# Kernel tuning notes

Hardware: AMD Instinct MI355X
Metric: run time of the kernel (lower is better)

The kernel has to match this reference:

```python
import jax, jax.numpy as jnp
import numpy as np

N, E, D_IN, D_OUT = 50000, 800000, 128, 128


def setup_inputs() -> dict:
    key = jax.random.key(0)
    ks = jax.random.split(key, 16)
    # edges with no self-loops (add_remaining_self_loops then simply appends one loop per node)
    row = jax.random.randint(ks[0], (E,), 0, N, dtype=jnp.int32)
    off = jax.random.randint(ks[1], (E,), 1, N, dtype=jnp.int32)
    col = (row + off) % N
    edge_index = jnp.stack([row, col], axis=0)
    s_in = 1.0 / np.sqrt(D_IN)
    s_out = 1.0 / np.sqrt(D_OUT)
    u = lambda k, shape, s: jax.random.uniform(k, shape, jnp.float32, -s, s)
    return {
        "x": jax.random.normal(ks[2], (N, D_IN), jnp.float32),
        "edge_index": edge_index,
        "W_hp": u(ks[3], (D_OUT, D_IN), s_in), "b_hp": u(ks[4], (D_OUT,), s_in),
        "W_lp": u(ks[5], (D_OUT, D_IN), s_in), "b_lp": u(ks[6], (D_OUT,), s_in),
        "W_i": u(ks[7], (D_OUT, D_IN), s_in), "b_i": u(ks[8], (D_OUT,), s_in),
        "wlin_h": u(ks[9], (D_OUT,), s_out), "blin_h": u(ks[10], (), s_out),
        "wlin_l": u(ks[11], (D_OUT,), s_out), "blin_l": u(ks[12], (), s_out),
        "wlin_i": u(ks[13], (D_OUT,), s_out), "blin_i": u(ks[14], (), s_out),
    }


def reference(x, edge_index, W_hp, b_hp, W_lp, b_lp, W_i, b_i,
              wlin_h, blin_h, wlin_l, blin_l, wlin_i, blin_i):
    n = x.shape[0]
    row, col = edge_index[0], edge_index[1]
    loop = jnp.arange(n, dtype=row.dtype)
    rf = jnp.concatenate([row, loop])  # sources incl. self-loops
    cf = jnp.concatenate([col, loop])  # targets incl. self-loops
    w = jnp.ones(rf.shape[0], x.dtype)
    # symmetric GCN normalization: D^{-1/2} A_hat D^{-1/2}
    deg = jax.ops.segment_sum(w, cf, num_segments=n)
    dinv = jnp.where(deg > 0, deg ** -0.5, 0.0).astype(x.dtype)
    w = dinv[rf] * w * dinv[cf]

    def agg(h):  # out[i] = sum_j w_e * h[j] over edges j->i
        return jax.ops.segment_sum(w[:, None] * h[rf], cf, num_segments=n)

    h_hp = x @ W_hp.T + b_hp
    H_hp = jax.nn.relu(h_hp - agg(h_hp))          # high-pass
    h_lp = x @ W_lp.T + b_lp
    H_lp = jax.nn.relu(agg(h_lp))                 # low-pass
    H_i = jax.nn.relu(x @ W_i.T + b_i)            # identity

    a_h = jax.nn.sigmoid(H_hp @ wlin_h + blin_h)  # [N]
    a_l = jax.nn.sigmoid(H_lp @ wlin_l + blin_l)
    a_i = jax.nn.sigmoid(H_i @ wlin_i + blin_i)
    # diag(alpha) @ H == alpha[:, None] * H
    return a_h[:, None] * H_hp + a_l[:, None] * H_lp + a_i[:, None] * H_i
```

## Files before the change

kernel.cpp:

```cpp
#include <hip/hip_runtime.h>
#include <cstdint>
#include <cstddef>

#define DEV __device__ __forceinline__

typedef __bf16 bf16x8 __attribute__((ext_vector_type(8)));
typedef float f32x4 __attribute__((ext_vector_type(4)));
typedef unsigned short ushort8v __attribute__((ext_vector_type(8)));

DEV ushort f2b(float f) {
  uint u = __float_as_uint(f);
  return (ushort)((u + 0x7FFFu + ((u >> 16) & 1u)) >> 16);
}

DEV ushort4 cvt4(float4 v) {
  ushort4 o; o.x = f2b(v.x); o.y = f2b(v.y); o.z = f2b(v.z); o.w = f2b(v.w);
  return o;
}

DEV float4 shfl_xor4(float4 v, int m) {
  float4 r;
  r.x = __shfl_xor(v.x, m); r.y = __shfl_xor(v.y, m);
  r.z = __shfl_xor(v.z, m); r.w = __shfl_xor(v.w, m);
  return r;
}

DEV float4 unpack4(uint2 u) {
  float4 r;
  r.x = __uint_as_float(u.x << 16);
  r.y = __uint_as_float(u.x & 0xFFFF0000u);
  r.z = __uint_as_float(u.y << 16);
  r.w = __uint_as_float(u.y & 0xFFFF0000u);
  return r;
}

DEV void fma4(float4& a, float w, uint2 u) {
  float4 v = unpack4(u);
  a.x = fmaf(w, v.x, a.x); a.y = fmaf(w, v.y, a.y);
  a.z = fmaf(w, v.z, a.z); a.w = fmaf(w, v.w, a.w);
}

__global__ __launch_bounds__(256) void k_count_cvtw(
    const int* __restrict__ col, int* __restrict__ cnt, int E, int nCB,
    const float* __restrict__ W0, const float* __restrict__ W1,
    const float* __restrict__ W2, ushort* __restrict__ Wb) {
  int b = blockIdx.x;
  if (b >= nCB) {
    int mi = b - nCB;
    const float* src = (mi == 0) ? W0 : (mi == 1) ? W1 : W2;
    ushort* dst = Wb + mi * 16384;
    for (int i = threadIdx.x * 4; i < 16384; i += 1024)
      *(ushort4*)(dst + i) = cvt4(*(const float4*)(src + i));
    return;
  }
  int e = b * 256 + threadIdx.x;
  if (e < E) atomicAdd(&cnt[col[e]], 1);
}

__global__ __launch_bounds__(256) void k_scanA(const int* __restrict__ cnt,
                                               int* __restrict__ off,
                                               float* __restrict__ dinv,
                                               int* __restrict__ btot, int N) {
  __shared__ int ws[4];
  int t = threadIdx.x, ln = t & 63, wv = t >> 6;
  int i = blockIdx.x * 256 + t;
  int v = (i < N) ? cnt[i] : 0;
  int inc = v;
#pragma unroll
  for (int o = 1; o < 64; o <<= 1) {
    int u = __shfl_up(inc, o);
    if (ln >= o) inc += u;
  }
  if (ln == 63) ws[wv] = inc;
  __syncthreads();
  if (t == 0) {
    int s = 0;
#pragma unroll
    for (int w = 0; w < 4; ++w) { int tmp = ws[w]; ws[w] = s; s += tmp; }
  }
  __syncthreads();
  int excl = ws[wv] + inc - v;
  if (i < N) {
    off[i] = excl;
    dinv[i] = rsqrtf((float)v + 1.0f);
  }
  if (t == 255) btot[blockIdx.x] = excl + v;
}

__global__ __launch_bounds__(256) void k_scanBC(int* __restrict__ off,
                                                const int* __restrict__ btot,
                                                int* __restrict__ cursor,
                                                int N, int E, int NB) {
  __shared__ int ws[4];
  __shared__ int pre_sh[256];
  int t = threadIdx.x, ln = t & 63, wv = t >> 6;
  int v = (t < NB) ? btot[t] : 0;
  int inc = v;
#pragma unroll
  for (int o = 1; o < 64; o <<= 1) {
    int u = __shfl_up(inc, o);
    if (ln >= o) inc += u;
  }
  if (ln == 63) ws[wv] = inc;
  __syncthreads();
  if (t == 0) {
    int s = 0;
#pragma unroll
    for (int w = 0; w < 4; ++w) { int tmp = ws[w]; ws[w] = s; s += tmp; }
  }
  __syncthreads();
  pre_sh[t] = ws[wv] + inc - v;
  __syncthreads();
  int bpre = pre_sh[blockIdx.x];
  int i = blockIdx.x * 256 + t;
  if (i < N) {
    int o = off[i] + bpre;
    off[i] = o;
    cursor[i] = o;
  }
  if (blockIdx.x == 0 && t == 0) off[N] = E;
}

__global__ __launch_bounds__(256) void k_scatter(const int* __restrict__ ei,
                                                 const float* __restrict__ dinv,
                                                 int* __restrict__ cursor,
                                                 int2* __restrict__ edata, int E) {
  int e = blockIdx.x * 256 + threadIdx.x;
  if (e >= E) return;
  int s = ei[e], d = ei[E + e];
  float w = dinv[s] * dinv[d];
  int p = atomicAdd(&cursor[d], 1);
  int2 v; v.x = s; v.y = __float_as_int(w);
  edata[p] = v;
}

__global__ __launch_bounds__(512) void k_gemm_fused(
    const float* __restrict__ x, const ushort* __restrict__ Wb,
    const float* __restrict__ b_hp, const float* __restrict__ b_lp,
    const float* __restrict__ b_i,
    ushort* __restrict__ h_all, int N) {
  __shared__ ushort Wl[16384];
  int tid = (int)threadIdx.x, lane = tid & 63, wv = tid >> 6;
  int r = lane & 15, g = lane >> 4;
  int NT = N >> 4;
  int t = blockIdx.x * 8 + wv;
  bool active = t < NT;

  bf16x8 Af[4];
  if (active) {
    const float* xp = x + ((size_t)t * 16 + r) * 128 + g * 8;
#pragma unroll
    for (int kc = 0; kc < 4; ++kc) {
      float4 v0 = *(const float4*)(xp + kc * 32);
      float4 v1 = *(const float4*)(xp + kc * 32 + 4);
      ushort8v u;
      u[0] = f2b(v0.x); u[1] = f2b(v0.y); u[2] = f2b(v0.z); u[3] = f2b(v0.w);
      u[4] = f2b(v1.x); u[5] = f2b(v1.y); u[6] = f2b(v1.z); u[7] = f2b(v1.w);
      Af[kc] = __builtin_bit_cast(bf16x8, u);
    }
  }

  for (int m = 0; m < 3; ++m) {
    __syncthreads();
    for (int i = tid; i < 2048; i += 512) {
      int byte = i << 4;
      int row = byte >> 8;
      int swz = byte ^ ((row & 7) << 4);
      *(ushort8v*)((char*)Wl + swz) = *(const ushort8v*)(Wb + m * 16384 + (i << 3));
    }
    __syncthreads();
    if (!active) continue;
    const float* bias = (m == 0) ? b_hp : (m == 1) ? b_lp : b_i;
    f32x4 acc[8];
#pragma unroll
    for (int ct = 0; ct < 8; ++ct) {
      float bb = bias[ct * 16 + r];
      f32x4 c; c[0] = bb; c[1] = bb; c[2] = bb; c[3] = bb;
      acc[ct] = c;
    }
#pragma unroll
    for (int kc = 0; kc < 4; ++kc)
#pragma unroll
      for (int ct = 0; ct < 8; ++ct) {
        int row = ct * 16 + r;
        int byte = row * 256 + kc * 64 + g * 16;
        int swz = byte ^ ((row & 7) << 4);
        bf16x8 B = *(const bf16x8*)((const char*)Wl + swz);
        acc[ct] = __builtin_amdgcn_mfma_f32_16x16x32_bf16(Af[kc], B, acc[ct], 0, 0, 0);
      }
    ushort* op = h_all + (size_t)(t * 16 + g * 4) * 384 + m * 128 + r;
#pragma unroll
    for (int ct = 0; ct < 8; ++ct)
#pragma unroll
      for (int j = 0; j < 4; ++j) {
        float v = acc[ct][j];
        if (m == 2) v = fmaxf(v, 0.f);
        op[(size_t)j * 384 + ct * 16] = f2b(v);
      }
  }
}

__global__ __launch_bounds__(256) void k_agg_final(
    const ushort* __restrict__ h_all, const float* __restrict__ dinv,
    const int* __restrict__ off, const int2* __restrict__ edata,
    const float* __restrict__ wlh, const float* __restrict__ wll,
    const float* __restrict__ wli,
    const float* __restrict__ pbh, const float* __restrict__ pbl,
    const float* __restrict__ pbi,
    float* __restrict__ out, int N) {
  int wv = (int)threadIdx.x >> 6;
  int lane = (int)threadIdx.x & 63;
  int node = blockIdx.x * 4 + wv;
  if (node >= N) return;

  const ushort* hb = h_all + 4 * lane;
  int p0 = off[node], p1 = off[node + 1];

  float4 a0 = {0,0,0,0}, a1 = {0,0,0,0}, a2 = {0,0,0,0}, a3 = {0,0,0,0};
  int p = p0;
  for (; p + 4 <= p1; p += 4) {
    int2 e0 = edata[p], e1 = edata[p + 1], e2 = edata[p + 2], e3 = edata[p + 3];
    uint2 u0 = *(const uint2*)(const void*)(hb + (size_t)e0.x * 384);
    uint2 u1 = *(const uint2*)(const void*)(hb + (size_t)e1.x * 384);
    uint2 u2 = *(const uint2*)(const void*)(hb + (size_t)e2.x * 384);
    uint2 u3 = *(const uint2*)(const void*)(hb + (size_t)e3.x * 384);
    fma4(a0, __int_as_float(e0.y), u0);
    fma4(a1, __int_as_float(e1.y), u1);
    fma4(a2, __int_as_float(e2.y), u2);
    fma4(a3, __int_as_float(e3.y), u3);
  }
  for (; p < p1; ++p) {
    int2 e = edata[p];
    uint2 u = *(const uint2*)(const void*)(hb + (size_t)e.x * 384);
    fma4(a0, __int_as_float(e.y), u);
  }
  float4 own;
  own.x = (a0.x + a1.x) + (a2.x + a3.x);
  own.y = (a0.y + a1.y) + (a2.y + a3.y);
  own.z = (a0.z + a1.z) + (a2.z + a3.z);
  own.w = (a0.w + a1.w) + (a2.w + a3.w);

  float di = dinv[node], wself = di * di;
  float4 sv = unpack4(*(const uint2*)(const void*)(hb + (size_t)node * 384));
  own.x = fmaf(wself, sv.x, own.x); own.y = fmaf(wself, sv.y, own.y);
  own.z = fmaf(wself, sv.z, own.z); own.w = fmaf(wself, sv.w, own.w);

  float4 oth = shfl_xor4(own, 32);
  float4 svo = shfl_xor4(sv, 32);
  bool hpside = (lane < 32);
  float4 hpSelf, aggHp, aggLp;
  hpSelf.x = hpside ? sv.x : svo.x; hpSelf.y = hpside ? sv.y : svo.y;
  hpSelf.z = hpside ? sv.z : svo.z; hpSelf.w = hpside ? sv.w : svo.w;
  aggHp.x = hpside ? own.x : oth.x; aggHp.y = hpside ? own.y : oth.y;
  aggHp.z = hpside ? own.z : oth.z; aggHp.w = hpside ? own.w : oth.w;
  aggLp.x = hpside ? oth.x : own.x; aggLp.y = hpside ? oth.y : own.y;
  aggLp.z = hpside ? oth.z : own.z; aggLp.w = hpside ? oth.w : own.w;

  float4 Hh, Hl;
  Hh.x = fmaxf(hpSelf.x - aggHp.x, 0.f); Hh.y = fmaxf(hpSelf.y - aggHp.y, 0.f);
  Hh.z = fmaxf(hpSelf.z - aggHp.z, 0.f); Hh.w = fmaxf(hpSelf.w - aggHp.w, 0.f);
  Hl.x = fmaxf(aggLp.x, 0.f); Hl.y = fmaxf(aggLp.y, 0.f);
  Hl.z = fmaxf(aggLp.z, 0.f); Hl.w = fmaxf(aggLp.w, 0.f);

  int c4 = 4 * (lane & 31);
  float4 hi4 = unpack4(*(const uint2*)(const void*)(h_all + (size_t)node * 384 + 256 + c4));
  float4 wh = *(const float4*)(wlh + c4);
  float4 wl = *(const float4*)(wll + c4);
  float4 wi = *(const float4*)(wli + c4);

  float dh = Hh.x * wh.x + Hh.y * wh.y + Hh.z * wh.z + Hh.w * wh.w;
  float dl = Hl.x * wl.x + Hl.y * wl.y + Hl.z * wl.z + Hl.w * wl.w;
  float dd = hi4.x * wi.x + hi4.y * wi.y + hi4.z * wi.z + hi4.w * wi.w;
#pragma unroll
  for (int o = 32; o > 0; o >>= 1) {
    dh += __shfl_xor(dh, o);
    dl += __shfl_xor(dl, o);
    dd += __shfl_xor(dd, o);
  }
  float a_h = 1.f / (1.f + __expf(-(0.5f * dh + pbh[0])));
  float a_l = 1.f / (1.f + __expf(-(0.5f * dl + pbl[0])));
  float a_i = 1.f / (1.f + __expf(-(0.5f * dd + pbi[0])));

  if (hpside) {
    float4 o4;
    o4.x = a_h * Hh.x + a_l * Hl.x + a_i * hi4.x;
    o4.y = a_h * Hh.y + a_l * Hl.y + a_i * hi4.y;
    o4.z = a_h * Hh.z + a_l * Hl.z + a_i * hi4.z;
    o4.w = a_h * Hh.w + a_l * Hl.w + a_i * hi4.w;
    *(float4*)(out + (size_t)node * 128 + c4) = o4;
  }
}

extern "C" void kernel_launch(void* const* d_in, const int* in_sizes, int n_in,
                              void* d_out, int out_size, void* d_ws, size_t ws_size,
                              hipStream_t stream) {
  const float* x     = (const float*)d_in[0];
  const int*   ei    = (const int*)d_in[1];
  const float* W_hp  = (const float*)d_in[2];
  const float* b_hp  = (const float*)d_in[3];
  const float* W_lp  = (const float*)d_in[4];
  const float* b_lp  = (const float*)d_in[5];
  const float* W_i   = (const float*)d_in[6];
  const float* b_i   = (const float*)d_in[7];
  const float* wlh   = (const float*)d_in[8];
  const float* pbh   = (const float*)d_in[9];
  const float* wll   = (const float*)d_in[10];
  const float* pbl   = (const float*)d_in[11];
  const float* wli   = (const float*)d_in[12];
  const float* pbi   = (const float*)d_in[13];
  float* out = (float*)d_out;

  int N = in_sizes[0] / 128;
  int E = in_sizes[1] / 2;
  int NB = (N + 255) / 256;
  int nCB = (E + 255) / 256;

  ushort* h_all = (ushort*)d_ws;
  ushort* Wb    = h_all + (size_t)N * 384;
  int2*   edata = (int2*)(Wb + 3 * 16384);
  float*  dinv  = (float*)(edata + E);
  int*    cnt   = (int*)(dinv + N);
  int*    off   = cnt + N;
  int*    cursor= off + N + 1;
  int*    btot  = cursor + N;

  hipMemsetAsync(cnt, 0, sizeof(int) * N, stream);
  k_count_cvtw<<<nCB + 3, 256, 0, stream>>>(ei + E, cnt, E, nCB, W_hp, W_lp, W_i, Wb);
  k_scanA<<<NB, 256, 0, stream>>>(cnt, off, dinv, btot, N);
  k_scanBC<<<NB, 256, 0, stream>>>(off, btot, cursor, N, E, NB);
  k_scatter<<<(E + 255) / 256, 256, 0, stream>>>(ei, dinv, cursor, edata, E);
  k_gemm_fused<<<(N / 16 + 7) / 8, 512, 0, stream>>>(x, Wb, b_hp, b_lp, b_i, h_all, N);
  k_agg_final<<<(N + 3) / 4, 256, 0, stream>>>(
      h_all, dinv, off, edata, wlh, wll, wli, pbh, pbl, pbi, out, N);
}
```

Measured before the change: 264.9 us.

## Fold weight conversion and count zeroing into GEMM, unroll aggregation by eight

Each GEMM block now converts the fp32 weights to bf16 itself while staging them into shared memory, and the GEMM also zeroes the degree-count array. This removes the memset and the separate weight-conversion blocks, and the GEMM is moved to the front of the launch sequence. The aggregation loop is unrolled from four to eight edges per iteration with more accumulators, to keep more gathers in flight, and the wave index is made scalar with readfirstlane. In exchange, every GEMM block redoes the weight conversion, and the extra accumulators raise register pressure.

```diff
diff --git a/kernel.cpp b/kernel.cpp
--- a/kernel.cpp
+++ b/kernel.cpp
@@ -11,11 +11,6 @@
 DEV ushort f2b(float f) {
   uint u = __float_as_uint(f);
   return (ushort)((u + 0x7FFFu + ((u >> 16) & 1u)) >> 16);
-}
-
-DEV ushort4 cvt4(float4 v) {
-  ushort4 o; o.x = f2b(v.x); o.y = f2b(v.y); o.z = f2b(v.z); o.w = f2b(v.w);
-  return o;
 }
 
 DEV float4 shfl_xor4(float4 v, int m) {
@@ -40,20 +35,90 @@
   a.z = fmaf(w, v.z, a.z); a.w = fmaf(w, v.w, a.w);
 }
 
-__global__ __launch_bounds__(256) void k_count_cvtw(
-    const int* __restrict__ col, int* __restrict__ cnt, int E, int nCB,
+__global__ __launch_bounds__(512) void k_gemm_fused(
+    const float* __restrict__ x,
     const float* __restrict__ W0, const float* __restrict__ W1,
-    const float* __restrict__ W2, ushort* __restrict__ Wb) {
-  int b = blockIdx.x;
-  if (b >= nCB) {
-    int mi = b - nCB;
-    const float* src = (mi == 0) ? W0 : (mi == 1) ? W1 : W2;
-    ushort* dst = Wb + mi * 16384;
-    for (int i = threadIdx.x * 4; i < 16384; i += 1024)
-      *(ushort4*)(dst + i) = cvt4(*(const float4*)(src + i));
-    return;
-  }
-  int e = b * 256 + threadIdx.x;
+    const float* __restrict__ W2,
+    const float* __restrict__ b_hp, const float* __restrict__ b_lp,
+    const float* __restrict__ b_i,
+    ushort* __restrict__ h_all, int* __restrict__ cnt, int N) {
+  int tid = (int)threadIdx.x;
+  {
+    int gsz = (int)gridDim.x * 512;
+    for (int i = (int)blockIdx.x * 512 + tid; i < N; i += gsz) cnt[i] = 0;
+  }
+
+  __shared__ ushort Wl[16384];
+  int lane = tid & 63, wv = tid >> 6;
+  int r = lane & 15, g = lane >> 4;
+  int NT = N >> 4;
+  int t = blockIdx.x * 8 + wv;
+  bool active = t < NT;
+
+  bf16x8 Af[4];
+  if (active) {
+    const float* xp = x + ((size_t)t * 16 + r) * 128 + g * 8;
+#pragma unroll
+    for (int kc = 0; kc < 4; ++kc) {
+      float4 v0 = *(const float4*)(xp + kc * 32);
+      float4 v1 = *(const float4*)(xp + kc * 32 + 4);
+      ushort8v u;
+      u[0] = f2b(v0.x); u[1] = f2b(v0.y); u[2] = f2b(v0.z); u[3] = f2b(v0.w);
+      u[4] = f2b(v1.x); u[5] = f2b(v1.y); u[6] = f2b(v1.z); u[7] = f2b(v1.w);
+      Af[kc] = __builtin_bit_cast(bf16x8, u);
+    }
+  }
+
+  for (int m = 0; m < 3; ++m) {
+    const float* Wsrc = (m == 0) ? W0 : (m == 1) ? W1 : W2;
+    __syncthreads();
+    for (int i = tid; i < 2048; i += 512) {
+      int byte = i << 4;
+      int row = byte >> 8;
+      int swz = byte ^ ((row & 7) << 4);
+      const float* s = Wsrc + (i << 3);
+      float4 v0 = *(const float4*)s;
+      float4 v1 = *(const float4*)(s + 4);
+      ushort8v u;
+      u[0] = f2b(v0.x); u[1] = f2b(v0.y); u[2] = f2b(v0.z); u[3] = f2b(v0.w);
+      u[4] = f2b(v1.x); u[5] = f2b(v1.y); u[6] = f2b(v1.z); u[7] = f2b(v1.w);
+      *(ushort8v*)((char*)Wl + swz) = u;
+    }
+    __syncthreads();
+    if (!active) continue;
+    const float* bias = (m == 0) ? b_hp : (m == 1) ? b_lp : b_i;
+    f32x4 acc[8];
+#pragma unroll
+    for (int ct = 0; ct < 8; ++ct) {
+      float bb = bias[ct * 16 + r];
+      f32x4 c; c[0] = bb; c[1] = bb; c[2] = bb; c[3] = bb;
+      acc[ct] = c;
+    }
+#pragma unroll
+    for (int kc = 0; kc < 4; ++kc)
+#pragma unroll
+      for (int ct = 0; ct < 8; ++ct) {
+        int row = ct * 16 + r;
+        int byte = row * 256 + kc * 64 + g * 16;
+        int swz = byte ^ ((row & 7) << 4);
+        bf16x8 B = *(const bf16x8*)((const char*)Wl + swz);
+        acc[ct] = __builtin_amdgcn_mfma_f32_16x16x32_bf16(Af[kc], B, acc[ct], 0, 0, 0);
+      }
+    ushort* op = h_all + (size_t)(t * 16 + g * 4) * 384 + m * 128 + r;
+#pragma unroll
+    for (int ct = 0; ct < 8; ++ct)
+#pragma unroll
+      for (int j = 0; j < 4; ++j) {
+        float v = acc[ct][j];
+        if (m == 2) v = fmaxf(v, 0.f);
+        op[(size_t)j * 384 + ct * 16] = f2b(v);
+      }
+  }
+}
+
+__global__ __launch_bounds__(256) void k_count(const int* __restrict__ col,
+                                               int* __restrict__ cnt, int E) {
+  int e = blockIdx.x * 256 + threadIdx.x;
   if (e < E) atomicAdd(&cnt[col[e]], 1);
 }
 
@@ -134,72 +199,6 @@
   edata[p] = v;
 }
 
-__global__ __launch_bounds__(512) void k_gemm_fused(
-    const float* __restrict__ x, const ushort* __restrict__ Wb,
-    const float* __restrict__ b_hp, const float* __restrict__ b_lp,
-    const float* __restrict__ b_i,
-    ushort* __restrict__ h_all, int N) {
-  __shared__ ushort Wl[16384];
-  int tid = (int)threadIdx.x, lane = tid & 63, wv = tid >> 6;
-  int r = lane & 15, g = lane >> 4;
-  int NT = N >> 4;
-  int t = blockIdx.x * 8 + wv;
-  bool active = t < NT;
-
-  bf16x8 Af[4];
-  if (active) {
-    const float* xp = x + ((size_t)t * 16 + r) * 128 + g * 8;
-#pragma unroll
-    for (int kc = 0; kc < 4; ++kc) {
-      float4 v0 = *(const float4*)(xp + kc * 32);
-      float4 v1 = *(const float4*)(xp + kc * 32 + 4);
-      ushort8v u;
-      u[0] = f2b(v0.x); u[1] = f2b(v0.y); u[2] = f2b(v0.z); u[3] = f2b(v0.w);
-      u[4] = f2b(v1.x); u[5] = f2b(v1.y); u[6] = f2b(v1.z); u[7] = f2b(v1.w);
-      Af[kc] = __builtin_bit_cast(bf16x8, u);
-    }
-  }
-
-  for (int m = 0; m < 3; ++m) {
-    __syncthreads();
-    for (int i = tid; i < 2048; i += 512) {
-      int byte = i << 4;
-      int row = byte >> 8;
-      int swz = byte ^ ((row & 7) << 4);
-      *(ushort8v*)((char*)Wl + swz) = *(const ushort8v*)(Wb + m * 16384 + (i << 3));
-    }
-    __syncthreads();
-    if (!active) continue;
-    const float* bias = (m == 0) ? b_hp : (m == 1) ? b_lp : b_i;
-    f32x4 acc[8];
-#pragma unroll
-    for (int ct = 0; ct < 8; ++ct) {
-      float bb = bias[ct * 16 + r];
-      f32x4 c; c[0] = bb; c[1] = bb; c[2] = bb; c[3] = bb;
-      acc[ct] = c;
-    }
-#pragma unroll
-    for (int kc = 0; kc < 4; ++kc)
-#pragma unroll
-      for (int ct = 0; ct < 8; ++ct) {
-        int row = ct * 16 + r;
-        int byte = row * 256 + kc * 64 + g * 16;
-        int swz = byte ^ ((row & 7) << 4);
-        bf16x8 B = *(const bf16x8*)((const char*)Wl + swz);
-        acc[ct] = __builtin_amdgcn_mfma_f32_16x16x32_bf16(Af[kc], B, acc[ct], 0, 0, 0);
-      }
-    ushort* op = h_all + (size_t)(t * 16 + g * 4) * 384 + m * 128 + r;
-#pragma unroll
-    for (int ct = 0; ct < 8; ++ct)
-#pragma unroll
-      for (int j = 0; j < 4; ++j) {
-        float v = acc[ct][j];
-        if (m == 2) v = fmaxf(v, 0.f);
-        op[(size_t)j * 384 + ct * 16] = f2b(v);
-      }
-  }
-}
-
 __global__ __launch_bounds__(256) void k_agg_final(
     const ushort* __restrict__ h_all, const float* __restrict__ dinv,
     const int* __restrict__ off, const int2* __restrict__ edata,
@@ -208,7 +207,7 @@
     const float* __restrict__ pbh, const float* __restrict__ pbl,
     const float* __restrict__ pbi,
     float* __restrict__ out, int N) {
-  int wv = (int)threadIdx.x >> 6;
+  int wv = __builtin_amdgcn_readfirstlane((int)threadIdx.x >> 6);
   int lane = (int)threadIdx.x & 63;
   int node = blockIdx.x * 4 + wv;
   if (node >= N) return;
@@ -217,17 +216,27 @@
   int p0 = off[node], p1 = off[node + 1];
 
   float4 a0 = {0,0,0,0}, a1 = {0,0,0,0}, a2 = {0,0,0,0}, a3 = {0,0,0,0};
+  float4 a4 = {0,0,0,0}, a5 = {0,0,0,0}, a6 = {0,0,0,0}, a7 = {0,0,0,0};
   int p = p0;
-  for (; p + 4 <= p1; p += 4) {
-    int2 e0 = edata[p], e1 = edata[p + 1], e2 = edata[p + 2], e3 = edata[p + 3];
+  for (; p + 8 <= p1; p += 8) {
+    int2 e0 = edata[p],     e1 = edata[p + 1], e2 = edata[p + 2], e3 = edata[p + 3];
+    int2 e4 = edata[p + 4], e5 = edata[p + 5], e6 = edata[p + 6], e7 = edata[p + 7];
     uint2 u0 = *(const uint2*)(const void*)(hb + (size_t)e0.x * 384);
     uint2 u1 = *(const uint2*)(const void*)(hb + (size_t)e1.x * 384);
     uint2 u2 = *(const uint2*)(const void*)(hb + (size_t)e2.x * 384);
     uint2 u3 = *(const uint2*)(const void*)(hb + (size_t)e3.x * 384);
+    uint2 u4 = *(const uint2*)(const void*)(hb + (size_t)e4.x * 384);
+    uint2 u5 = *(const uint2*)(const void*)(hb + (size_t)e5.x * 384);
+    uint2 u6 = *(const uint2*)(const void*)(hb + (size_t)e6.x * 384);
+    uint2 u7 = *(const uint2*)(const void*)(hb + (size_t)e7.x * 384);
     fma4(a0, __int_as_float(e0.y), u0);
     fma4(a1, __int_as_float(e1.y), u1);
     fma4(a2, __int_as_float(e2.y), u2);
     fma4(a3, __int_as_float(e3.y), u3);
+    fma4(a4, __int_as_float(e4.y), u4);
+    fma4(a5, __int_as_float(e5.y), u5);
+    fma4(a6, __int_as_float(e6.y), u6);
+    fma4(a7, __int_as_float(e7.y), u7);
   }
   for (; p < p1; ++p) {
     int2 e = edata[p];
@@ -235,10 +244,10 @@
     fma4(a0, __int_as_float(e.y), u);
   }
   float4 own;
-  own.x = (a0.x + a1.x) + (a2.x + a3.x);
-  own.y = (a0.y + a1.y) + (a2.y + a3.y);
-  own.z = (a0.z + a1.z) + (a2.z + a3.z);
-  own.w = (a0.w + a1.w) + (a2.w + a3.w);
+  own.x = ((a0.x + a1.x) + (a2.x + a3.x)) + ((a4.x + a5.x) + (a6.x + a7.x));
+  own.y = ((a0.y + a1.y) + (a2.y + a3.y)) + ((a4.y + a5.y) + (a6.y + a7.y));
+  own.z = ((a0.z + a1.z) + (a2.z + a3.z)) + ((a4.z + a5.z) + (a6.z + a7.z));
+  own.w = ((a0.w + a1.w) + (a2.w + a3.w)) + ((a4.w + a5.w) + (a6.w + a7.w));
 
   float di = dinv[node], wself = di * di;
   float4 sv = unpack4(*(const uint2*)(const void*)(hb + (size_t)node * 384));
@@ -313,23 +322,21 @@
   int N = in_sizes[0] / 128;
   int E = in_sizes[1] / 2;
   int NB = (N + 255) / 256;
-  int nCB = (E + 255) / 256;
 
   ushort* h_all = (ushort*)d_ws;
-  ushort* Wb    = h_all + (size_t)N * 384;
-  int2*   edata = (int2*)(Wb + 3 * 16384);
+  int2*   edata = (int2*)(h_all + (size_t)N * 384);
   float*  dinv  = (float*)(edata + E);
   int*    cnt   = (int*)(dinv + N);
   int*    off   = cnt + N;
   int*    cursor= off + N + 1;
   int*    btot  = cursor + N;
 
-  hipMemsetAsync(cnt, 0, sizeof(int) * N, stream);
-  k_count_cvtw<<<nCB + 3, 256, 0, stream>>>(ei + E, cnt, E, nCB, W_hp, W_lp, W_i, Wb);
+  k_gemm_fused<<<(N / 16 + 7) / 8, 512, 0, stream>>>(
+      x, W_hp, W_lp, W_i, b_hp, b_lp, b_i, h_all, cnt, N);
+  k_count<<<(E + 255) / 256, 256, 0, stream>>>(ei + E, cnt, E);
   k_scanA<<<NB, 256, 0, stream>>>(cnt, off, dinv, btot, N);
   k_scanBC<<<NB, 256, 0, stream>>>(off, btot, cursor, N, E, NB);
   k_scatter<<<(E + 255) / 256, 256, 0, stream>>>(ei, dinv, cursor, edata, E);
-  k_gemm_fused<<<(N / 16 + 7) / 8, 512, 0, stream>>>(x, Wb, b_hp, b_lp, b_i, h_all, N);
   k_agg_final<<<(N + 3) / 4, 256, 0, stream>>>(
       h_all, dinv, off, edata, wlh, wll, wli, pbh, pbl, pbi, out, N);
 }
```

Result: no change. 260.8 us (-1.5%).
